# Kernel tuning notes

Measured on AMD Instinct MI355X. Metric: run time of the kernel, lower is better.

Reference implementation:

```python
import jax, jax.numpy as jnp
import numpy as np

SEQ_LEN = 128
INPUT_DIM = 256
HIDDEN_DIM = 1024
NUM_CLASSES = 10
BATCH = 1024


def setup_inputs() -> dict:
    key = jax.random.key(0)
    ks = jax.random.split(key, 12)
    D, H, C = INPUT_DIM, HIDDEN_DIM, NUM_CLASSES
    s = 0.02
    return {
        "x": jax.random.randint(ks[0], (BATCH, SEQ_LEN), 0, SEQ_LEN),
        "embed_w": jax.random.normal(ks[1], (SEQ_LEN, D), dtype=jnp.float32),
        "w_g": jax.random.normal(ks[2], (H, D + H), dtype=jnp.float32) * s,
        "w_i": jax.random.normal(ks[3], (H, D + H), dtype=jnp.float32) * s,
        "w_f": jax.random.normal(ks[4], (H, D + H), dtype=jnp.float32) * s,
        "w_o": jax.random.normal(ks[5], (H, D + H), dtype=jnp.float32) * s,
        "b_g": jax.random.normal(ks[6], (H,), dtype=jnp.float32) * s,
        "b_i": jax.random.normal(ks[7], (H,), dtype=jnp.float32) * s,
        "b_f": jax.random.normal(ks[8], (H,), dtype=jnp.float32) * s,
        "b_o": jax.random.normal(ks[9], (H,), dtype=jnp.float32) * s,
        "w_p": jax.random.normal(ks[10], (C, H), dtype=jnp.float32) * s,
        "b_p": jax.random.normal(ks[11], (C,), dtype=jnp.float32) * s,
    }


def reference(x, embed_w, w_g, w_i, w_f, w_o, b_g, b_i, b_f, b_o, w_p, b_p):
    B = x.shape[0]
    H = w_g.shape[0]
    embeds = embed_w[x]  # [B, S, D]
    h0 = jnp.zeros((B, H), dtype=embed_w.dtype)
    c0 = jnp.zeros((B, H), dtype=embed_w.dtype)

    # Faithful to the original, which calls cell_forward(t, h, c) against a
    # signature (x, c, h) and assigns h, c = (new_c, new_h).
    def step(carry, xt):
        h, c = carry
        x_h = jnp.concatenate([xt, c], axis=1)  # original concats x with its 'h' param == c
        g = jnp.tanh(x_h @ w_g.T + b_g)
        i = jax.nn.sigmoid(x_h @ w_i.T + b_i)
        f = jax.nn.sigmoid(x_h @ w_f.T + b_f)
        o = jax.nn.sigmoid(x_h @ w_o.T + b_o)
        new_c = g * i + h * f  # original's 'c' param == h
        new_h = jnp.tanh(new_c) * o
        return (new_c, new_h), None  # assigned back as h, c = new_c, new_h

    (h, c), _ = jax.lax.scan(step, (h0, c0), jnp.transpose(embeds, (1, 0, 2)))
    return jax.nn.softmax(h @ w_p.T + b_p, axis=1)
```

## Files before the change

### kernel.cpp

```cpp
#include <hip/hip_runtime.h>
#include <hip/hip_bf16.h>


typedef __attribute__((ext_vector_type(8))) short bf16x8;
typedef __attribute__((ext_vector_type(4))) float f32x4;

#define GLOBAL_AS __attribute__((address_space(1)))
#define LDS_AS    __attribute__((address_space(3)))

static __device__ __forceinline__ void async_copy16(const void* g, void* l) {
    __builtin_amdgcn_global_load_lds((const GLOBAL_AS void*)g, (LDS_AS void*)l, 16, 0, 0);
}
static __device__ __forceinline__ float sigm(float x) {
    return 1.f / (1.f + __expf(-x));
}
static __device__ __forceinline__ float tanh_fast(float x) {
    return 1.f - 2.f / (__expf(2.f * x) + 1.f);
}

__global__ __launch_bounds__(256) void prep_table(
    const float* __restrict__ embed,
    const float* __restrict__ wg, const float* __restrict__ wi,
    const float* __restrict__ wf, const float* __restrict__ wo,
    const float* __restrict__ bg, const float* __restrict__ bi,
    const float* __restrict__ bff, const float* __restrict__ bo,
    float* __restrict__ T)
{
    __shared__ float e[8][256];
    const int tid = threadIdx.x;
    const int col = blockIdx.x * 256 + tid;
    const int s0 = blockIdx.y * 8;
    const int j = col >> 2, g = col & 3;
    const float* w = (g == 0 ? wg : g == 1 ? wi : g == 2 ? wf : wo) + (size_t)j * 1280;
    const float bias = (g == 0 ? bg : g == 1 ? bi : g == 2 ? bff : bo)[j];
    #pragma unroll
    for (int i = 0; i < 8; ++i) e[i][tid] = embed[(s0 + i) * 256 + tid];
    __syncthreads();
    const float4* w4 = (const float4*)w;
    float acc[8];
    #pragma unroll
    for (int i = 0; i < 8; ++i) acc[i] = bias;
    for (int d = 0; d < 64; ++d) {
        const float4 wv = w4[d];
        #pragma unroll
        for (int i = 0; i < 8; ++i) {
            const float4 ev = ((const float4*)e[i])[d];
            acc[i] += ev.x * wv.x + ev.y * wv.y + ev.z * wv.z + ev.w * wv.w;
        }
    }
    #pragma unroll
    for (int i = 0; i < 8; ++i)
        T[(size_t)(s0 + i) * 4096 + col] = acc[i];
}

__global__ __launch_bounds__(256) void pack_w(
    const float* __restrict__ wg, const float* __restrict__ wi,
    const float* __restrict__ wf, const float* __restrict__ wo,
    __hip_bfloat16* __restrict__ Wt)
{
    const int col = blockIdx.x;
    const int j = col >> 2, g = col & 3;
    const float* w = (g == 0 ? wg : g == 1 ? wi : g == 2 ? wf : wo)
                     + (size_t)j * 1280 + 256;
    __hip_bfloat16* out = Wt + (size_t)col * 1024;
    for (int k = threadIdx.x; k < 1024; k += 256)
        out[k] = __float2bfloat16(w[k]);
}

__global__ __launch_bounds__(512, 4) void step_fused(
    const __hip_bfloat16* __restrict__ Wt,
    const float* __restrict__ T,
    const int* __restrict__ X,
    const __hip_bfloat16* __restrict__ Hprev,
    __hip_bfloat16* __restrict__ Hnext,
    float* __restrict__ CSblob,
    float* __restrict__ CSout,
    int t)
{
    __shared__ char lds[2][24576];
    const int tid = threadIdx.x;
    const int w = tid >> 6, l = tid & 63;
    const int wm = w >> 1, wn = w & 1;
    const int wcol0 = (blockIdx.x & 31) * 128;
    const int batch0 = (blockIdx.x >> 5) * 64;

#define STAGE(K0, BUF) do {                                                    \
        _Pragma("unroll")                                                      \
        for (int i_ = 0; i_ < 2; ++i_) {                                       \
            const int sW = tid + i_ * 512;                                     \
            const int rW = sW >> 3, cW = sW & 7;                               \
            async_copy16(Wt + (size_t)(wcol0 + rW) * 1024 + (K0)               \
                             + ((cW ^ (rW & 7)) << 3),                         \
                         &lds[BUF][sW * 16]);                                  \
        }                                                                      \
        const int sH = tid;                                                    \
        const int rH = sH >> 3, cH = sH & 7;                                   \
        async_copy16(Hprev + (size_t)(batch0 + rH) * 1024 + (K0)               \
                         + ((cH ^ (rH & 7)) << 3),                             \
                     &lds[BUF][16384 + sH * 16]);                              \
    } while (0)

    int batchN[2], jM[2];
    #pragma unroll
    for (int n = 0; n < 2; ++n) batchN[n] = batch0 + wn * 32 + n * 16 + (l & 15);
    #pragma unroll
    for (int m = 0; m < 2; ++m) jM[m] = (wcol0 >> 2) + wm * 8 + m * 4 + (l >> 4);

    f32x4 tv[2][2];
    float ap[2][2];
    #pragma unroll
    for (int n = 0; n < 2; ++n) {
        const int s = X[batchN[n] * 128 + t];
        #pragma unroll
        for (int m = 0; m < 2; ++m)
            tv[m][n] = *(const f32x4*)&T[(size_t)s * 4096 + jM[m] * 4];
    }
    float* blob = CSblob + ((size_t)blockIdx.x * 512 + tid) * 4;
    if (t > 0) {
        #pragma unroll
        for (int m = 0; m < 2; ++m)
            #pragma unroll
            for (int n = 0; n < 2; ++n) ap[m][n] = blob[m * 2 + n];
    } else {
        #pragma unroll
        for (int m = 0; m < 2; ++m)
            #pragma unroll
            for (int n = 0; n < 2; ++n) ap[m][n] = 0.f;
    }
    asm volatile("s_waitcnt vmcnt(0)" ::: "memory");

    STAGE(0, 0);
    asm volatile("s_waitcnt vmcnt(0)" ::: "memory");
    __builtin_amdgcn_s_barrier();

    f32x4 acc[2][2];
    const f32x4 z4 = {0.f, 0.f, 0.f, 0.f};
    #pragma unroll
    for (int m = 0; m < 2; ++m)
        #pragma unroll
        for (int n = 0; n < 2; ++n) acc[m][n] = z4;

    #pragma unroll
    for (int kt = 0; kt < 16; ++kt) {
        if (kt < 15) STAGE((kt + 1) * 64, (kt + 1) & 1);
        if (kt == 15)     asm volatile("s_waitcnt vmcnt(0)" ::: "memory");
        else if (kt > 0)  asm volatile("s_waitcnt vmcnt(3)" ::: "memory");
        if (kt > 0) __builtin_amdgcn_s_barrier();

        const char* base = &lds[kt & 1][0];
        #pragma unroll
        for (int kk = 0; kk < 2; ++kk) {
            bf16x8 af[2], bfr[2];
            #pragma unroll
            for (int m = 0; m < 2; ++m) {
                const int row = wm * 32 + m * 16 + (l & 15);
                const int ch = (kk * 4 + (l >> 4)) ^ (row & 7);
                af[m] = *(const bf16x8*)(base + (row * 8 + ch) * 16);
            }
            #pragma unroll
            for (int n = 0; n < 2; ++n) {
                const int row = wn * 32 + n * 16 + (l & 15);
                const int ch = (kk * 4 + (l >> 4)) ^ (row & 7);
                bfr[n] = *(const bf16x8*)(base + 16384 + (row * 8 + ch) * 16);
            }
            #pragma unroll
            for (int m = 0; m < 2; ++m)
                #pragma unroll
                for (int n = 0; n < 2; ++n)
                    acc[m][n] = __builtin_amdgcn_mfma_f32_16x16x32_bf16(
                        af[m], bfr[n], acc[m][n], 0, 0, 0);
        }
        if (kt < 15) __builtin_amdgcn_s_barrier();
    }
#undef STAGE

    #pragma unroll
    for (int m = 0; m < 2; ++m)
        #pragma unroll
        for (int n = 0; n < 2; ++n) {
            const float z0 = acc[m][n][0] + tv[m][n][0];
            const float z1 = acc[m][n][1] + tv[m][n][1];
            const float z2 = acc[m][n][2] + tv[m][n][2];
            const float z3 = acc[m][n][3] + tv[m][n][3];
            const float gg = tanh_fast(z0);
            const float ii = sigm(z1);
            const float ff = sigm(z2);
            const float oo = sigm(z3);
            const float na = gg * ii + ap[m][n] * ff;
            blob[m * 2 + n] = na;
            Hnext[(size_t)batchN[n] * 1024 + jM[m]] =
                __float2bfloat16(tanh_fast(na) * oo);
            if (t == 127)
                CSout[(size_t)batchN[n] * 1024 + jM[m]] = na;
        }
}

__global__ __launch_bounds__(256) void proj_softmax(
    const float* __restrict__ A,
    const float* __restrict__ Wp,
    const float* __restrict__ bp,
    float* __restrict__ out)
{
    const int row = blockIdx.x;
    const float* a = A + (size_t)row * 1024;
    float p[10];
    #pragma unroll
    for (int c = 0; c < 10; ++c) p[c] = 0.f;
    for (int k = threadIdx.x; k < 1024; k += 256) {
        const float av = a[k];
        #pragma unroll
        for (int c = 0; c < 10; ++c) p[c] += av * Wp[c * 1024 + k];
    }
    #pragma unroll
    for (int c = 0; c < 10; ++c)
        #pragma unroll
        for (int off = 32; off; off >>= 1) p[c] += __shfl_down(p[c], off);
    __shared__ float red[4][10];
    const int wv = threadIdx.x >> 6, ln = threadIdx.x & 63;
    if (ln == 0)
        for (int c = 0; c < 10; ++c) red[wv][c] = p[c];
    __syncthreads();
    if (threadIdx.x == 0) {
        float logits[10], mx = -1e30f;
        for (int c = 0; c < 10; ++c) {
            logits[c] = red[0][c] + red[1][c] + red[2][c] + red[3][c] + bp[c];
            mx = fmaxf(mx, logits[c]);
        }
        float sum = 0.f;
        for (int c = 0; c < 10; ++c) { logits[c] = __expf(logits[c] - mx); sum += logits[c]; }
        const float inv = 1.f / sum;
        for (int c = 0; c < 10; ++c) out[(size_t)row * 10 + c] = logits[c] * inv;
    }
}

extern "C" void kernel_launch(void* const* d_in, const int* in_sizes, int n_in,
                              void* d_out, int out_size, void* d_ws, size_t ws_size,
                              hipStream_t stream) {
    (void)in_sizes; (void)n_in; (void)out_size; (void)ws_size;
    const int*   x     = (const int*)d_in[0];
    const float* embed = (const float*)d_in[1];
    const float* wg    = (const float*)d_in[2];
    const float* wi    = (const float*)d_in[3];
    const float* wf    = (const float*)d_in[4];
    const float* wo    = (const float*)d_in[5];
    const float* bg    = (const float*)d_in[6];
    const float* bi    = (const float*)d_in[7];
    const float* bff   = (const float*)d_in[8];
    const float* bo    = (const float*)d_in[9];
    const float* wp    = (const float*)d_in[10];
    const float* bp    = (const float*)d_in[11];
    float* out = (float*)d_out;

    char* ws = (char*)d_ws;
    float*          T    = (float*)(ws);
    __hip_bfloat16* Wt   = (__hip_bfloat16*)(ws + (2u << 20));
    __hip_bfloat16* BhA  = (__hip_bfloat16*)(ws + (10u << 20));
    __hip_bfloat16* BhB  = (__hip_bfloat16*)(ws + (12u << 20));
    float*          CSo  = (float*)(ws + (14u << 20));
    float*          CSb  = (float*)(ws + (18u << 20));

    prep_table<<<dim3(16, 16), 256, 0, stream>>>(embed, wg, wi, wf, wo, bg, bi, bff, bo, T);
    pack_w<<<4096, 256, 0, stream>>>(wg, wi, wf, wo, Wt);
    hipMemsetAsync(BhA, 0, (size_t)1024 * 1024 * sizeof(__hip_bfloat16), stream);

    for (int t = 0; t < 128; ++t) {
        const __hip_bfloat16* Hp = (t & 1) ? BhB : BhA;
        __hip_bfloat16*       Hn = (t & 1) ? BhA : BhB;
        step_fused<<<512, 512, 0, stream>>>(Wt, T, x, Hp, Hn, CSb, CSo, t);
    }
    proj_softmax<<<1024, 256, 0, stream>>>(CSo, wp, bp, out);
}
```

Baseline: 2.249 ms.

## Use 128x128 tiles with 32x32 MFMA and split-K across wave pairs

Each step kernel block now computes a 128-column by 128-batch tile instead of 128 by 64, which halves the grid to 256 blocks. It uses the 32x32x16 bf16 MFMA and stages 64KB per LDS buffer. Each pair of waves splits the K dimension into two halves and reduces its partial accumulators through LDS before the gate epilogue, with the gate-bias table load moved after the GEMM. The aim is more operand reuse and fewer global loads per FLOP. The cost is higher LDS use, lower occupancy, an extra reduction pass, and fewer blocks than there are CUs.

```diff
diff --git a/kernel.cpp b/kernel.cpp
--- a/kernel.cpp
+++ b/kernel.cpp
@@ -4,6 +4,7 @@
 
 typedef __attribute__((ext_vector_type(8))) short bf16x8;
 typedef __attribute__((ext_vector_type(4))) float f32x4;
+typedef __attribute__((ext_vector_type(16))) float f32x16;
 
 #define GLOBAL_AS __attribute__((address_space(1)))
 #define LDS_AS    __attribute__((address_space(3)))
@@ -67,7 +68,7 @@
         out[k] = __float2bfloat16(w[k]);
 }
 
-__global__ __launch_bounds__(512, 4) void step_fused(
+__global__ __launch_bounds__(512, 2) void step_fused(
     const __hip_bfloat16* __restrict__ Wt,
     const float* __restrict__ T,
     const int* __restrict__ X,
@@ -77,121 +78,147 @@
     float* __restrict__ CSout,
     int t)
 {
-    __shared__ char lds[2][24576];
+    __shared__ char lds[2][65536];
     const int tid = threadIdx.x;
     const int w = tid >> 6, l = tid & 63;
-    const int wm = w >> 1, wn = w & 1;
+    const int h = w & 1;
+    const int p = w >> 1;
+    const int pm = p >> 1, pn = p & 1;
     const int wcol0 = (blockIdx.x & 31) * 128;
-    const int batch0 = (blockIdx.x >> 5) * 64;
-
-#define STAGE(K0, BUF) do {                                                    \
-        _Pragma("unroll")                                                      \
-        for (int i_ = 0; i_ < 2; ++i_) {                                       \
-            const int sW = tid + i_ * 512;                                     \
-            const int rW = sW >> 3, cW = sW & 7;                               \
-            async_copy16(Wt + (size_t)(wcol0 + rW) * 1024 + (K0)               \
-                             + ((cW ^ (rW & 7)) << 3),                         \
-                         &lds[BUF][sW * 16]);                                  \
-        }                                                                      \
-        const int sH = tid;                                                    \
-        const int rH = sH >> 3, cH = sH & 7;                                   \
-        async_copy16(Hprev + (size_t)(batch0 + rH) * 1024 + (K0)               \
-                         + ((cH ^ (rH & 7)) << 3),                             \
-                     &lds[BUF][16384 + sH * 16]);                              \
+    const int batch0 = (blockIdx.x >> 5) * 128;
+    const int hi = l >> 5, lr = l & 31;
+
+#define STAGE(BUF, KT) do {                                                  \
+        _Pragma("unroll")                                                    \
+        for (int tau = 0; tau < 4; ++tau) {                                  \
+            _Pragma("unroll")                                                \
+            for (int i_ = 0; i_ < 2; ++i_) {                                 \
+                const int s_ = tid + i_ * 512;                               \
+                const int r_ = s_ >> 3, c_ = s_ & 7;                         \
+                const int kq_ = (tau & 1) * 512 + (KT) * 64                  \
+                                + ((c_ ^ (r_ & 7)) << 3);                    \
+                const __hip_bfloat16* src_ = (tau < 2)                       \
+                    ? Wt + (size_t)(wcol0 + r_) * 1024 + kq_                 \
+                    : Hprev + (size_t)(batch0 + r_) * 1024 + kq_;            \
+                async_copy16(src_, &lds[BUF][tau * 16384 + s_ * 16]);        \
+            }                                                                \
+        }                                                                    \
     } while (0)
 
-    int batchN[2], jM[2];
-    #pragma unroll
-    for (int n = 0; n < 2; ++n) batchN[n] = batch0 + wn * 32 + n * 16 + (l & 15);
-    #pragma unroll
-    for (int m = 0; m < 2; ++m) jM[m] = (wcol0 >> 2) + wm * 8 + m * 4 + (l >> 4);
-
-    f32x4 tv[2][2];
-    float ap[2][2];
-    #pragma unroll
-    for (int n = 0; n < 2; ++n) {
-        const int s = X[batchN[n] * 128 + t];
-        #pragma unroll
-        for (int m = 0; m < 2; ++m)
-            tv[m][n] = *(const f32x4*)&T[(size_t)s * 4096 + jM[m] * 4];
-    }
-    float* blob = CSblob + ((size_t)blockIdx.x * 512 + tid) * 4;
+    int batchN[2];
+    #pragma unroll
+    for (int n = 0; n < 2; ++n) batchN[n] = batch0 + pn * 64 + n * 32 + lr;
+    int sN[2];
+    #pragma unroll
+    for (int n = 0; n < 2; ++n) sN[n] = X[batchN[n] * 128 + t];
+
+    float* blob = CSblob + ((size_t)blockIdx.x * 512 + tid) * 8;
+    float ap[8];
     if (t > 0) {
-        #pragma unroll
-        for (int m = 0; m < 2; ++m)
-            #pragma unroll
-            for (int n = 0; n < 2; ++n) ap[m][n] = blob[m * 2 + n];
+        f32x4 b0 = *(const f32x4*)&blob[0];
+        f32x4 b1 = *(const f32x4*)&blob[4];
+        #pragma unroll
+        for (int c = 0; c < 4; ++c) { ap[c] = b0[c]; ap[4 + c] = b1[c]; }
     } else {
         #pragma unroll
-        for (int m = 0; m < 2; ++m)
-            #pragma unroll
-            for (int n = 0; n < 2; ++n) ap[m][n] = 0.f;
-    }
-    asm volatile("s_waitcnt vmcnt(0)" ::: "memory");
+        for (int c = 0; c < 8; ++c) ap[c] = 0.f;
+    }
 
     STAGE(0, 0);
     asm volatile("s_waitcnt vmcnt(0)" ::: "memory");
     __builtin_amdgcn_s_barrier();
 
-    f32x4 acc[2][2];
-    const f32x4 z4 = {0.f, 0.f, 0.f, 0.f};
-    #pragma unroll
-    for (int m = 0; m < 2; ++m)
-        #pragma unroll
-        for (int n = 0; n < 2; ++n) acc[m][n] = z4;
-
-    #pragma unroll
-    for (int kt = 0; kt < 16; ++kt) {
-        if (kt < 15) STAGE((kt + 1) * 64, (kt + 1) & 1);
-        if (kt == 15)     asm volatile("s_waitcnt vmcnt(0)" ::: "memory");
-        else if (kt > 0)  asm volatile("s_waitcnt vmcnt(3)" ::: "memory");
-        if (kt > 0) __builtin_amdgcn_s_barrier();
-
-        const char* base = &lds[kt & 1][0];
-        #pragma unroll
-        for (int kk = 0; kk < 2; ++kk) {
+    f32x16 acc[2][2];
+    #pragma unroll
+    for (int i = 0; i < 2; ++i)
+        #pragma unroll
+        for (int n = 0; n < 2; ++n)
+            #pragma unroll
+            for (int c = 0; c < 16; ++c) acc[i][n][c] = 0.f;
+
+    #pragma unroll
+    for (int kt = 0; kt < 8; ++kt) {
+        if (kt < 7) STAGE((kt + 1) & 1, kt + 1);
+        if (kt > 0) {
+            if (kt == 7) asm volatile("s_waitcnt vmcnt(0)" ::: "memory");
+            else         asm volatile("s_waitcnt vmcnt(8)" ::: "memory");
+            __builtin_amdgcn_s_barrier();
+        }
+        const char* wb = &lds[kt & 1][h * 16384];
+        const char* hb = &lds[kt & 1][32768 + h * 16384];
+        #pragma unroll
+        for (int kk = 0; kk < 4; ++kk) {
             bf16x8 af[2], bfr[2];
             #pragma unroll
-            for (int m = 0; m < 2; ++m) {
-                const int row = wm * 32 + m * 16 + (l & 15);
-                const int ch = (kk * 4 + (l >> 4)) ^ (row & 7);
-                af[m] = *(const bf16x8*)(base + (row * 8 + ch) * 16);
+            for (int i = 0; i < 2; ++i) {
+                const int row = pm * 64 + ((h ^ i) << 5) + lr;
+                const int ch = (kk * 2 + hi) ^ (row & 7);
+                af[i] = *(const bf16x8*)(wb + (row * 8 + ch) * 16);
             }
             #pragma unroll
             for (int n = 0; n < 2; ++n) {
-                const int row = wn * 32 + n * 16 + (l & 15);
-                const int ch = (kk * 4 + (l >> 4)) ^ (row & 7);
-                bfr[n] = *(const bf16x8*)(base + 16384 + (row * 8 + ch) * 16);
+                const int row = pn * 64 + (n << 5) + lr;
+                const int ch = (kk * 2 + hi) ^ (row & 7);
+                bfr[n] = *(const bf16x8*)(hb + (row * 8 + ch) * 16);
             }
             #pragma unroll
-            for (int m = 0; m < 2; ++m)
+            for (int i = 0; i < 2; ++i)
                 #pragma unroll
                 for (int n = 0; n < 2; ++n)
-                    acc[m][n] = __builtin_amdgcn_mfma_f32_16x16x32_bf16(
-                        af[m], bfr[n], acc[m][n], 0, 0, 0);
-        }
-        if (kt < 15) __builtin_amdgcn_s_barrier();
+                    acc[i][n] = __builtin_amdgcn_mfma_f32_32x32x16_bf16(
+                        af[i], bfr[n], acc[i][n], 0, 0, 0);
+        }
+        if (kt < 7) __builtin_amdgcn_s_barrier();
     }
 #undef STAGE
 
-    #pragma unroll
-    for (int m = 0; m < 2; ++m)
-        #pragma unroll
-        for (int n = 0; n < 2; ++n) {
-            const float z0 = acc[m][n][0] + tv[m][n][0];
-            const float z1 = acc[m][n][1] + tv[m][n][1];
-            const float z2 = acc[m][n][2] + tv[m][n][2];
-            const float z3 = acc[m][n][3] + tv[m][n][3];
+    float* red = (float*)&lds[0][0];
+    #pragma unroll
+    for (int n = 0; n < 2; ++n)
+        #pragma unroll
+        for (int q = 0; q < 4; ++q) {
+            const int u = ((1 - h) * 2 + n) * 4 + q;
+            f32x4 v = { acc[1][n][q * 4 + 0], acc[1][n][q * 4 + 1],
+                        acc[1][n][q * 4 + 2], acc[1][n][q * 4 + 3] };
+            *(f32x4*)&red[p * 4096 + (l * 16 + (u ^ (l & 15))) * 4] = v;
+        }
+    __syncthreads();
+    #pragma unroll
+    for (int n = 0; n < 2; ++n)
+        #pragma unroll
+        for (int q = 0; q < 4; ++q) {
+            const int u = (h * 2 + n) * 4 + q;
+            const f32x4 v = *(const f32x4*)&red[p * 4096 + (l * 16 + (u ^ (l & 15))) * 4];
+            #pragma unroll
+            for (int g = 0; g < 4; ++g) acc[0][n][q * 4 + g] += v[g];
+        }
+
+    const int jbase = (wcol0 >> 2) + pm * 16 + h * 8;
+    f32x4 tvv[2][4];
+    #pragma unroll
+    for (int n = 0; n < 2; ++n)
+        #pragma unroll
+        for (int q = 0; q < 4; ++q)
+            tvv[n][q] = *(const f32x4*)&T[(size_t)sN[n] * 4096 + (jbase + q * 2 + hi) * 4];
+
+    #pragma unroll
+    for (int n = 0; n < 2; ++n)
+        #pragma unroll
+        for (int q = 0; q < 4; ++q) {
+            const int j = jbase + q * 2 + hi;
+            const float z0 = acc[0][n][q * 4 + 0] + tvv[n][q][0];
+            const float z1 = acc[0][n][q * 4 + 1] + tvv[n][q][1];
+            const float z2 = acc[0][n][q * 4 + 2] + tvv[n][q][2];
+            const float z3 = acc[0][n][q * 4 + 3] + tvv[n][q][3];
             const float gg = tanh_fast(z0);
             const float ii = sigm(z1);
             const float ff = sigm(z2);
             const float oo = sigm(z3);
-            const float na = gg * ii + ap[m][n] * ff;
-            blob[m * 2 + n] = na;
-            Hnext[(size_t)batchN[n] * 1024 + jM[m]] =
-                __float2bfloat16(tanh_fast(na) * oo);
+            const float na = gg * ii + ap[n * 4 + q] * ff;
+            blob[n * 4 + q] = na;
+            Hnext[(size_t)batchN[n] * 1024 + j] = __float2bfloat16(tanh_fast(na) * oo);
             if (t == 127)
-                CSout[(size_t)batchN[n] * 1024 + jM[m]] = na;
+                CSout[(size_t)batchN[n] * 1024 + j] = na;
         }
 }
 
@@ -266,7 +293,7 @@
     for (int t = 0; t < 128; ++t) {
         const __hip_bfloat16* Hp = (t & 1) ? BhB : BhA;
         __hip_bfloat16*       Hn = (t & 1) ? BhA : BhB;
-        step_fused<<<512, 512, 0, stream>>>(Wt, T, x, Hp, Hn, CSb, CSo, t);
+        step_fused<<<256, 512, 0, stream>>>(Wt, T, x, Hp, Hn, CSb, CSo, t);
     }
     proj_softmax<<<1024, 256, 0, stream>>>(CSo, wp, bp, out);
 }
```

Measured after the change: 2.416 ms. +7.4%, slower.

## Triple-buffer LDS staging with depth-two prefetch and one barrier per k-step

Applied to the files above, without the earlier changes.

Moves from a double-buffered LDS pipeline with two barriers per k-iteration to a triple-buffered one. The first two K tiles are issued before the table and state loads, and each iteration then prefetches two tiles ahead after a single barrier. All LDS fragments for both k-halves are loaded before the MFMA burst, which runs under raised wave priority (s_setprio). The aim is to hide global-load latency and cut barrier stalls in each recurrent step. The cost is 72KB of LDS per block instead of 48KB, which lowers how many blocks can be resident per CU.

```diff
diff --git a/kernel.cpp b/kernel.cpp
--- a/kernel.cpp
+++ b/kernel.cpp
@@ -77,7 +77,7 @@
     float* __restrict__ CSout,
     int t)
 {
-    __shared__ char lds[2][24576];
+    __shared__ char lds[3][24576];
     const int tid = threadIdx.x;
     const int w = tid >> 6, l = tid & 63;
     const int wm = w >> 1, wn = w & 1;
@@ -100,6 +100,9 @@
                      &lds[BUF][16384 + sH * 16]);                              \
     } while (0)
 
+    STAGE(0, 0);
+    STAGE(64, 1);
+
     int batchN[2], jM[2];
     #pragma unroll
     for (int n = 0; n < 2; ++n) batchN[n] = batch0 + wn * 32 + n * 16 + (l & 15);
@@ -127,11 +130,6 @@
             #pragma unroll
             for (int n = 0; n < 2; ++n) ap[m][n] = 0.f;
     }
-    asm volatile("s_waitcnt vmcnt(0)" ::: "memory");
-
-    STAGE(0, 0);
-    asm volatile("s_waitcnt vmcnt(0)" ::: "memory");
-    __builtin_amdgcn_s_barrier();
 
     f32x4 acc[2][2];
     const f32x4 z4 = {0.f, 0.f, 0.f, 0.f};
@@ -142,35 +140,43 @@
 
     #pragma unroll
     for (int kt = 0; kt < 16; ++kt) {
-        if (kt < 15) STAGE((kt + 1) * 64, (kt + 1) & 1);
-        if (kt == 15)     asm volatile("s_waitcnt vmcnt(0)" ::: "memory");
-        else if (kt > 0)  asm volatile("s_waitcnt vmcnt(3)" ::: "memory");
-        if (kt > 0) __builtin_amdgcn_s_barrier();
-
-        const char* base = &lds[kt & 1][0];
-        #pragma unroll
-        for (int kk = 0; kk < 2; ++kk) {
-            bf16x8 af[2], bfr[2];
-            #pragma unroll
-            for (int m = 0; m < 2; ++m) {
-                const int row = wm * 32 + m * 16 + (l & 15);
-                const int ch = (kk * 4 + (l >> 4)) ^ (row & 7);
-                af[m] = *(const bf16x8*)(base + (row * 8 + ch) * 16);
-            }
-            #pragma unroll
-            for (int n = 0; n < 2; ++n) {
-                const int row = wn * 32 + n * 16 + (l & 15);
-                const int ch = (kk * 4 + (l >> 4)) ^ (row & 7);
-                bfr[n] = *(const bf16x8*)(base + 16384 + (row * 8 + ch) * 16);
-            }
-            #pragma unroll
-            for (int m = 0; m < 2; ++m)
-                #pragma unroll
-                for (int n = 0; n < 2; ++n)
-                    acc[m][n] = __builtin_amdgcn_mfma_f32_16x16x32_bf16(
-                        af[m], bfr[n], acc[m][n], 0, 0, 0);
-        }
-        if (kt < 15) __builtin_amdgcn_s_barrier();
+        if (kt == 15) asm volatile("s_waitcnt vmcnt(0)" ::: "memory");
+        else          asm volatile("s_waitcnt vmcnt(3)" ::: "memory");
+        __builtin_amdgcn_s_barrier();
+        if (kt < 14) STAGE((kt + 2) * 64, (kt + 2) % 3);
+
+        const char* base = &lds[kt % 3][0];
+        bf16x8 af0[2], bfr0[2], af1[2], bfr1[2];
+        #pragma unroll
+        for (int m = 0; m < 2; ++m) {
+            const int row = wm * 32 + m * 16 + (l & 15);
+            const int ch0 = (l >> 4) ^ (row & 7);
+            const int ch1 = (4 + (l >> 4)) ^ (row & 7);
+            af0[m] = *(const bf16x8*)(base + (row * 8 + ch0) * 16);
+            af1[m] = *(const bf16x8*)(base + (row * 8 + ch1) * 16);
+        }
+        #pragma unroll
+        for (int n = 0; n < 2; ++n) {
+            const int row = wn * 32 + n * 16 + (l & 15);
+            const int ch0 = (l >> 4) ^ (row & 7);
+            const int ch1 = (4 + (l >> 4)) ^ (row & 7);
+            bfr0[n] = *(const bf16x8*)(base + 16384 + (row * 8 + ch0) * 16);
+            bfr1[n] = *(const bf16x8*)(base + 16384 + (row * 8 + ch1) * 16);
+        }
+        __builtin_amdgcn_s_setprio(1);
+        #pragma unroll
+        for (int m = 0; m < 2; ++m)
+            #pragma unroll
+            for (int n = 0; n < 2; ++n)
+                acc[m][n] = __builtin_amdgcn_mfma_f32_16x16x32_bf16(
+                    af0[m], bfr0[n], acc[m][n], 0, 0, 0);
+        #pragma unroll
+        for (int m = 0; m < 2; ++m)
+            #pragma unroll
+            for (int n = 0; n < 2; ++n)
+                acc[m][n] = __builtin_amdgcn_mfma_f32_16x16x32_bf16(
+                    af1[m], bfr1[n], acc[m][n], 0, 0, 0);
+        __builtin_amdgcn_s_setprio(0);
     }
 #undef STAGE
 
```

Result: faster. 2.158 ms (-4.0%).

## Double batch tile per block, enlarge per-wave MFMA tile, defer table loads

Applied to the files above, without the earlier changes.

Each block now covers 128 batch rows instead of 64 and launches 256 blocks instead of 512. Each wave computes a 64x32 output tile with 8 MFMAs per k-step, so every weight tile loaded into LDS is reused across twice as many batch rows, halving weight global traffic per step. The gate-table and X lookups move after the GEMM to cut register pressure, and s_setprio is raised around the MFMA bursts. In exchange, LDS per block grows to 64KB, only 256 blocks fill the 256 CUs (one wave-group per CU), and the epilogue loads are no longer overlapped with the GEMM.

```diff
diff --git a/kernel.cpp b/kernel.cpp
--- a/kernel.cpp
+++ b/kernel.cpp
@@ -77,66 +77,46 @@
     float* __restrict__ CSout,
     int t)
 {
-    __shared__ char lds[2][24576];
+    __shared__ char lds[2][32768];
     const int tid = threadIdx.x;
     const int w = tid >> 6, l = tid & 63;
-    const int wm = w >> 1, wn = w & 1;
+    const int wm = w >> 2, wn = w & 3;
     const int wcol0 = (blockIdx.x & 31) * 128;
-    const int batch0 = (blockIdx.x >> 5) * 64;
+    const int batch0 = (blockIdx.x >> 5) * 128;
 
 #define STAGE(K0, BUF) do {                                                    \
         _Pragma("unroll")                                                      \
         for (int i_ = 0; i_ < 2; ++i_) {                                       \
-            const int sW = tid + i_ * 512;                                     \
-            const int rW = sW >> 3, cW = sW & 7;                               \
-            async_copy16(Wt + (size_t)(wcol0 + rW) * 1024 + (K0)               \
-                             + ((cW ^ (rW & 7)) << 3),                         \
-                         &lds[BUF][sW * 16]);                                  \
+            const int s_ = tid + i_ * 512;                                     \
+            const int r_ = s_ >> 3, c_ = s_ & 7;                               \
+            const int kq_ = (K0) + ((c_ ^ (r_ & 7)) << 3);                     \
+            async_copy16(Wt + (size_t)(wcol0 + r_) * 1024 + kq_,               \
+                         &lds[BUF][s_ * 16]);                                  \
+            async_copy16(Hprev + (size_t)(batch0 + r_) * 1024 + kq_,           \
+                         &lds[BUF][16384 + s_ * 16]);                          \
         }                                                                      \
-        const int sH = tid;                                                    \
-        const int rH = sH >> 3, cH = sH & 7;                                   \
-        async_copy16(Hprev + (size_t)(batch0 + rH) * 1024 + (K0)               \
-                         + ((cH ^ (rH & 7)) << 3),                             \
-                     &lds[BUF][16384 + sH * 16]);                              \
     } while (0)
 
-    int batchN[2], jM[2];
-    #pragma unroll
-    for (int n = 0; n < 2; ++n) batchN[n] = batch0 + wn * 32 + n * 16 + (l & 15);
-    #pragma unroll
-    for (int m = 0; m < 2; ++m) jM[m] = (wcol0 >> 2) + wm * 8 + m * 4 + (l >> 4);
-
-    f32x4 tv[2][2];
-    float ap[2][2];
-    #pragma unroll
-    for (int n = 0; n < 2; ++n) {
-        const int s = X[batchN[n] * 128 + t];
-        #pragma unroll
-        for (int m = 0; m < 2; ++m)
-            tv[m][n] = *(const f32x4*)&T[(size_t)s * 4096 + jM[m] * 4];
-    }
-    float* blob = CSblob + ((size_t)blockIdx.x * 512 + tid) * 4;
+    float* blob = CSblob + ((size_t)blockIdx.x * 512 + tid) * 8;
+    float ap[8];
     if (t > 0) {
-        #pragma unroll
-        for (int m = 0; m < 2; ++m)
-            #pragma unroll
-            for (int n = 0; n < 2; ++n) ap[m][n] = blob[m * 2 + n];
+        f32x4 b0 = *(const f32x4*)&blob[0];
+        f32x4 b1 = *(const f32x4*)&blob[4];
+        #pragma unroll
+        for (int c = 0; c < 4; ++c) { ap[c] = b0[c]; ap[4 + c] = b1[c]; }
     } else {
         #pragma unroll
-        for (int m = 0; m < 2; ++m)
-            #pragma unroll
-            for (int n = 0; n < 2; ++n) ap[m][n] = 0.f;
-    }
-    asm volatile("s_waitcnt vmcnt(0)" ::: "memory");
+        for (int c = 0; c < 8; ++c) ap[c] = 0.f;
+    }
 
     STAGE(0, 0);
     asm volatile("s_waitcnt vmcnt(0)" ::: "memory");
     __builtin_amdgcn_s_barrier();
 
-    f32x4 acc[2][2];
+    f32x4 acc[4][2];
     const f32x4 z4 = {0.f, 0.f, 0.f, 0.f};
     #pragma unroll
-    for (int m = 0; m < 2; ++m)
+    for (int m = 0; m < 4; ++m)
         #pragma unroll
         for (int n = 0; n < 2; ++n) acc[m][n] = z4;
 
@@ -144,16 +124,16 @@
     for (int kt = 0; kt < 16; ++kt) {
         if (kt < 15) STAGE((kt + 1) * 64, (kt + 1) & 1);
         if (kt == 15)     asm volatile("s_waitcnt vmcnt(0)" ::: "memory");
-        else if (kt > 0)  asm volatile("s_waitcnt vmcnt(3)" ::: "memory");
+        else if (kt > 0)  asm volatile("s_waitcnt vmcnt(4)" ::: "memory");
         if (kt > 0) __builtin_amdgcn_s_barrier();
 
         const char* base = &lds[kt & 1][0];
         #pragma unroll
         for (int kk = 0; kk < 2; ++kk) {
-            bf16x8 af[2], bfr[2];
+            bf16x8 af[4], bfr[2];
             #pragma unroll
-            for (int m = 0; m < 2; ++m) {
-                const int row = wm * 32 + m * 16 + (l & 15);
+            for (int m = 0; m < 4; ++m) {
+                const int row = wm * 64 + m * 16 + (l & 15);
                 const int ch = (kk * 4 + (l >> 4)) ^ (row & 7);
                 af[m] = *(const bf16x8*)(base + (row * 8 + ch) * 16);
             }
@@ -163,36 +143,48 @@
                 const int ch = (kk * 4 + (l >> 4)) ^ (row & 7);
                 bfr[n] = *(const bf16x8*)(base + 16384 + (row * 8 + ch) * 16);
             }
+            __builtin_amdgcn_s_setprio(1);
             #pragma unroll
-            for (int m = 0; m < 2; ++m)
+            for (int m = 0; m < 4; ++m)
                 #pragma unroll
                 for (int n = 0; n < 2; ++n)
                     acc[m][n] = __builtin_amdgcn_mfma_f32_16x16x32_bf16(
                         af[m], bfr[n], acc[m][n], 0, 0, 0);
+            __builtin_amdgcn_s_setprio(0);
         }
         if (kt < 15) __builtin_amdgcn_s_barrier();
     }
 #undef STAGE
 
-    #pragma unroll
-    for (int m = 0; m < 2; ++m)
-        #pragma unroll
-        for (int n = 0; n < 2; ++n) {
-            const float z0 = acc[m][n][0] + tv[m][n][0];
-            const float z1 = acc[m][n][1] + tv[m][n][1];
-            const float z2 = acc[m][n][2] + tv[m][n][2];
-            const float z3 = acc[m][n][3] + tv[m][n][3];
+    int batchN[2], jM[4];
+    #pragma unroll
+    for (int n = 0; n < 2; ++n) batchN[n] = batch0 + wn * 32 + n * 16 + (l & 15);
+    #pragma unroll
+    for (int m = 0; m < 4; ++m) jM[m] = (wcol0 >> 2) + wm * 16 + m * 4 + (l >> 4);
+
+    #pragma unroll
+    for (int n = 0; n < 2; ++n) {
+        const int s = X[batchN[n] * 128 + t];
+        const float* Ts = T + (size_t)s * 4096;
+        #pragma unroll
+        for (int m = 0; m < 4; ++m) {
+            const f32x4 tv = *(const f32x4*)&Ts[jM[m] * 4];
+            const float z0 = acc[m][n][0] + tv[0];
+            const float z1 = acc[m][n][1] + tv[1];
+            const float z2 = acc[m][n][2] + tv[2];
+            const float z3 = acc[m][n][3] + tv[3];
             const float gg = tanh_fast(z0);
             const float ii = sigm(z1);
             const float ff = sigm(z2);
             const float oo = sigm(z3);
-            const float na = gg * ii + ap[m][n] * ff;
+            const float na = gg * ii + ap[m * 2 + n] * ff;
             blob[m * 2 + n] = na;
             Hnext[(size_t)batchN[n] * 1024 + jM[m]] =
                 __float2bfloat16(tanh_fast(na) * oo);
             if (t == 127)
                 CSout[(size_t)batchN[n] * 1024 + jM[m]] = na;
         }
+    }
 }
 
 __global__ __launch_bounds__(256) void proj_softmax(
@@ -266,7 +258,7 @@
     for (int t = 0; t < 128; ++t) {
         const __hip_bfloat16* Hp = (t & 1) ? BhB : BhA;
         __hip_bfloat16*       Hn = (t & 1) ? BhA : BhB;
-        step_fused<<<512, 512, 0, stream>>>(Wt, T, x, Hp, Hn, CSb, CSo, t);
+        step_fused<<<256, 512, 0, stream>>>(Wt, T, x, Hp, Hn, CSb, CSo, t);
     }
     proj_softmax<<<1024, 256, 0, stream>>>(CSo, wp, bp, out);
 }
```

Measured after the change: 2.236 ms. About the same (-0.6%).
